# Kernel tuning notes

Hardware: AMD Instinct MI355X
Metric: run time of the kernel (lower is better)

Reference implementation:

```python
import jax, jax.numpy as jnp
import numpy as np

N = 50000
NEG_SLOPE = 0.2


def leaky_relu(x, slope=NEG_SLOPE):
    return jnp.where(x >= 0, x, slope * x)


def gat_conv(x, edge_index, W, a_src, a_dst, bias):
    """PyG GATConv, heads=1, add_self_loops=True.
    x: [N, Fin], edge_index: [2, E] (row 0 = source j, row 1 = target i),
    W: [Fin, Fout], a_src/a_dst: [Fout], bias: [Fout].
    """
    n = x.shape[0]
    # add self loops
    loops = jnp.arange(n, dtype=edge_index.dtype)
    src = jnp.concatenate([edge_index[0], loops])
    dst = jnp.concatenate([edge_index[1], loops])

    xw = x @ W                       # [N, Fout]
    alpha_src = xw @ a_src           # [N]
    alpha_dst = xw @ a_dst           # [N]

    e = leaky_relu(alpha_src[src] + alpha_dst[dst])   # [E+N]
    # segment softmax over edges sharing the same target node
    m = jax.ops.segment_max(e, dst, num_segments=n)   # [N]
    ex = jnp.exp(e - m[dst])
    denom = jax.ops.segment_sum(ex, dst, num_segments=n)  # [N] (>0 via self loops)
    att = ex / denom[dst]                              # [E+N]

    msgs = att[:, None] * xw[src]                      # [E+N, Fout]
    out = jax.ops.segment_sum(msgs, dst, num_segments=n)
    return out + bias


def setup_inputs() -> dict:
    key = jax.random.key(0)
    ks = jax.random.split(key, 12)
    E = 800000
    Fin, H, Fout = 128, 256, 128
    x = jax.random.normal(ks[0], (N, Fin), dtype=jnp.float32)
    edge_index = jax.random.randint(ks[1], (2, E), 0, N, dtype=jnp.int64)
    s = 0.1
    W1 = jax.random.normal(ks[2], (Fin, H), dtype=jnp.float32) * s
    a1_src = jax.random.normal(ks[3], (H,), dtype=jnp.float32) * s
    a1_dst = jax.random.normal(ks[4], (H,), dtype=jnp.float32) * s
    b1 = jax.random.normal(ks[5], (H,), dtype=jnp.float32) * s
    W2 = jax.random.normal(ks[6], (H, Fout), dtype=jnp.float32) * s
    a2_src = jax.random.normal(ks[7], (Fout,), dtype=jnp.float32) * s
    a2_dst = jax.random.normal(ks[8], (Fout,), dtype=jnp.float32) * s
    b2 = jax.random.normal(ks[9], (Fout,), dtype=jnp.float32) * s
    return {"x": x, "edge_index": edge_index, "W1": W1, "a1_src": a1_src,
            "a1_dst": a1_dst, "b1": b1, "W2": W2, "a2_src": a2_src,
            "a2_dst": a2_dst, "b2": b2}


def reference(x, edge_index, W1, a1_src, a1_dst, b1, W2, a2_src, a2_dst, b2):
    h = jax.nn.relu(gat_conv(x, edge_index, W1, a1_src, a1_dst, b1))
    return gat_conv(h, edge_index, W2, a2_src, a2_dst, b2)
```

## Files before the change

### kernel.cpp

```cpp
#include <hip/hip_runtime.h>
#include <hip/hip_bf16.h>

typedef __attribute__((ext_vector_type(8))) short short8;
typedef __attribute__((ext_vector_type(4))) float floatx4;

#define CAP 8192
#define BIN_CH 2048
#define NPB 16

__device__ __forceinline__ float read_f(const void* p, long long i, int fp32m) {
  return fp32m ? ((const float*)p)[i] : (float)((const __hip_bfloat16*)p)[i];
}
__device__ __forceinline__ float bf2f(unsigned short u) {
  return __uint_as_float((unsigned)u << 16);
}
__device__ __forceinline__ unsigned short f2bf(float f) {
  const unsigned u = __float_as_uint(f);
  return (unsigned short)((u + 0x7fffu + ((u >> 16) & 1u)) >> 16);
}

__device__ __forceinline__ void pack_one(const void* W, unsigned short* Wp, int i,
                                         int K, int NOUT, int m) {
  const int k = i / NOUT, n = i - k * NOUT;
  const int ct = n >> 4, c = n & 15, ks = k >> 5, quad = (k >> 3) & 3, j = k & 7;
  Wp[(((ct * (K / 32) + ks) * 4 + quad) * 16 + c) * 8 + j] = f2bf(read_f(W, i, m));
}

__global__ __launch_bounds__(256) void prep_k(const void* __restrict__ x,
                                              const void* __restrict__ ei,
                                              const void* __restrict__ W1,
                                              const void* __restrict__ a1s,
                                              const void* __restrict__ a1d,
                                              const void* __restrict__ b1,
                                              const void* __restrict__ W2,
                                              const void* __restrict__ a2s,
                                              const void* __restrict__ a2d,
                                              const void* __restrict__ b2,
                                              unsigned short* __restrict__ Wp1,
                                              unsigned short* __restrict__ Wp2,
                                              float* __restrict__ w_as1, float* __restrict__ w_ad1,
                                              float* __restrict__ v_a2s, float* __restrict__ v_a2d,
                                              float* __restrict__ v_b1,  float* __restrict__ v_b2,
                                              int* __restrict__ bkcnt,
                                              int* __restrict__ flags) {
  __shared__ int fl_s[2];
  const int t = threadIdx.x, b = blockIdx.x;
  if (t < 64) {
    const unsigned short w = ((const unsigned short*)x)[t * 2];
    const int ef = (w >> 7) & 0xff;
    const bool bf_ok = (ef >= 90 && ef <= 140);
    const unsigned hi = ((const unsigned*)ei)[t * 2 + 1];
    const unsigned long long bm = __ballot(bf_ok);
    const unsigned long long zm = __ballot(hi == 0u);
    if (t == 0) {
      fl_s[0] = (bm == ~0ull) ? 0 : 1;
      fl_s[1] = (zm == ~0ull) ? 1 : 0;
      if (b == 0) { flags[0] = fl_s[0]; flags[1] = fl_s[1]; }
    }
  }
  __syncthreads();
  const int m = fl_s[0];

  if (b < 128) {
    pack_one(W1, Wp1, b * 256 + t, 128, 256, m);
  } else if (b < 256) {
    pack_one(W2, Wp2, (b - 128) * 256 + t, 256, 128, m);
  } else if (b == 256) {
    if (t < 128) {
      float sa = 0.f, sb = 0.f;
      for (int j = 0; j < 256; ++j) {
        const float w = read_f(W1, (long long)t * 256 + j, m);
        sa = fmaf(w, read_f(a1s, j, m), sa);
        sb = fmaf(w, read_f(a1d, j, m), sb);
      }
      w_as1[t] = sa;
      w_ad1[t] = sb;
    }
  } else if (b == 257) {
    if (t < 128) v_a2s[t] = read_f(a2s, t, m);
    else         v_a2d[t - 128] = read_f(a2d, t - 128, m);
  } else if (b == 258) {
    v_b1[t] = read_f(b1, t, m);
  } else {
    if (t < 128) v_b2[t] = read_f(b2, t, m);
    bkcnt[t] = 0;
  }
}

__device__ __forceinline__ void edge_sd(const void* ei, int e, int E, int i64m, int n,
                                        int& s, int& d) {
  if (e < E) {
    if (i64m) { s = (int)((const long long*)ei)[e]; d = (int)((const long long*)ei)[E + e]; }
    else      { s = ((const int*)ei)[e];            d = ((const int*)ei)[E + e]; }
  } else { s = d = e - E; }
  s = min(max(s, 0), n - 1);
  d = min(max(d, 0), n - 1);
}

__global__ __launch_bounds__(256) void front2_k(const void* __restrict__ x,
                                                const void* __restrict__ ei,
                                                const float* __restrict__ w_as1,
                                                const float* __restrict__ w_ad1,
                                                unsigned short* __restrict__ xb,
                                                float* __restrict__ as_, float* __restrict__ ad_,
                                                unsigned* __restrict__ bpool,
                                                int* __restrict__ bkcnt,
                                                int n, int E, int EN, int nbc) {
  __shared__ int fl_s[2];
  __shared__ unsigned stage[BIN_CH];
  __shared__ unsigned daddr[BIN_CH];
  __shared__ int shA[256], shB[256], shC[256], shD[256];
  __shared__ int vtot_s;
  const int t = threadIdx.x, b = blockIdx.x;

  if (t < 64) {
    const unsigned short w = ((const unsigned short*)x)[t * 2];
    const int ef = (w >> 7) & 0xff;
    const bool bf_ok = (ef >= 90 && ef <= 140);
    const unsigned hi = ((const unsigned*)ei)[t * 2 + 1];
    const unsigned long long bm = __ballot(bf_ok);
    const unsigned long long zm = __ballot(hi == 0u);
    if (t == 0) {
      fl_s[0] = (bm == ~0ull) ? 0 : 1;
      fl_s[1] = (zm == ~0ull) ? 1 : 0;
    }
  }
  __syncthreads();
  const int m = fl_s[0], i64m = fl_s[1];

  if (b < nbc) {
    const int gid = b * 256 + t;
    const int node = gid >> 6, lane = gid & 63;
    if (node >= n) return;
    const long long base = (long long)node * 128 + lane * 2;
    const float v0 = read_f(x, base, m), v1 = read_f(x, base + 1, m);
    ushort2 q;
    q.x = f2bf(v0); q.y = f2bf(v1);
    *(ushort2*)(xb + base) = q;
    float s1 = fmaf(v0, w_as1[lane * 2], v1 * w_as1[lane * 2 + 1]);
    float s2 = fmaf(v0, w_ad1[lane * 2], v1 * w_ad1[lane * 2 + 1]);
    for (int off = 32; off; off >>= 1) {
      s1 += __shfl_down(s1, off);
      s2 += __shfl_down(s2, off);
    }
    if (lane == 0) { as_[node] = s1; ad_[node] = s2; }
  } else {
    const int c0 = (b - nbc) * BIN_CH;
    int* bcnt_s = shA; int* boff_s = shB; int* gbase_s = shC; int* sd = shD;
    bcnt_s[t] = 0;
    __syncthreads();

    unsigned val[BIN_CH / 256];
    int buk[BIN_CH / 256];
#pragma unroll
    for (int i = 0; i < BIN_CH / 256; ++i) {
      const int e = c0 + i * 256 + t;
      if (e < EN) {
        int s, d;
        edge_sd(ei, e, E, i64m, n, s, d);
        buk[i] = d >> 8;
        val[i] = (unsigned)s | ((unsigned)(d & 255) << 16);
        atomicAdd(&bcnt_s[buk[i]], 1);
      } else buk[i] = -1;
    }
    __syncthreads();

    const int c = bcnt_s[t];
    sd[t] = c;
    __syncthreads();
    for (int off = 1; off < 256; off <<= 1) {
      const int v = (t >= off) ? sd[t - off] : 0;
      __syncthreads();
      sd[t] += v;
      __syncthreads();
    }
    boff_s[t] = sd[t] - c;
    if (t == 255) vtot_s = sd[255];
    gbase_s[t] = (c > 0) ? atomicAdd(&bkcnt[t], c) : 0;
    bcnt_s[t] = 0;
    __syncthreads();

#pragma unroll
    for (int i = 0; i < BIN_CH / 256; ++i) {
      if (buk[i] >= 0) {
        const int lp = atomicAdd(&bcnt_s[buk[i]], 1);
        const int si = boff_s[buk[i]] + lp;
        stage[si] = val[i];
        const int gp = gbase_s[buk[i]] + lp;
        daddr[si] = (gp < CAP) ? (unsigned)(buk[i] * CAP + gp) : 0xFFFFFFFFu;
      }
    }
    __syncthreads();

    const int vt = vtot_s;
    for (int idx = t; idx < vt; idx += 256)
      if (daddr[idx] != 0xFFFFFFFFu) bpool[daddr[idx]] = stage[idx];
  }
}

__global__ __launch_bounds__(1024) void bucket_csr_k(const unsigned* __restrict__ bpool,
                                                     const int* __restrict__ bkcnt,
                                                     unsigned short* __restrict__ csrc,
                                                     int* __restrict__ start_g,
                                                     int* __restrict__ deg_g, int n) {
  __shared__ int deg_s[256], cur_s[256], sd[256];
  const int t = threadIdx.x, b = blockIdx.x;
  int cnt = bkcnt[b];
  if (cnt > CAP) cnt = CAP;
  if (t < 256) deg_s[t] = 0;
  __syncthreads();
  for (int idx = t; idx < cnt; idx += 1024) {
    const unsigned v = bpool[b * CAP + idx];
    atomicAdd(&deg_s[(v >> 16) & 255], 1);
  }
  __syncthreads();
  const int dg = (t < 256) ? deg_s[t] : 0;
  if (t < 256) sd[t] = dg;
  __syncthreads();
  for (int off = 1; off < 256; off <<= 1) {
    const int v = (t < 256 && t >= off) ? sd[t - off] : 0;
    __syncthreads();
    if (t < 256) sd[t] += v;
    __syncthreads();
  }
  if (t < 256) {
    const int excl = sd[t] - dg;
    const int node = b * 256 + t;
    if (node < n) { start_g[node] = b * CAP + excl; deg_g[node] = dg; }
    cur_s[t] = excl;
  }
  __syncthreads();
  for (int idx = t; idx < cnt; idx += 1024) {
    const unsigned v = bpool[b * CAP + idx];
    const int p = atomicAdd(&cur_s[(v >> 16) & 255], 1);
    csrc[b * CAP + p] = (unsigned short)(v & 0xFFFFu);
  }
}

__device__ __forceinline__ void agg_node(const int start, const int end,
                                         const unsigned short* __restrict__ csrc,
                                         const float* __restrict__ as_, const float adv,
                                         const unsigned short* __restrict__ xw,
                                         const int lane, float* acc) {
  const int slot = lane >> 4, col = lane & 15;
  float dsum = 0.f;
#pragma unroll
  for (int c = 0; c < 8; ++c) acc[c] = 0.f;

  for (int base = start; base < end; base += 64) {
    const int idx = base + lane;
    int s_pre = 0;
    float w_pre = 0.f;
    if (idx < end) {
      s_pre = (int)csrc[idx];
      float v = as_[s_pre] + adv;
      v = (v >= 0.f) ? v : 0.2f * v;
      w_pre = __expf(fminf(v, 60.f));
    }
    dsum += w_pre;
    const int cnt = min(64, end - base);
    for (int j = 0; j < cnt; j += 8) {
      const int jj0 = j + slot, jj1 = j + 4 + slot;
      int s0 = __shfl(s_pre, jj0);
      float w0 = __shfl(w_pre, jj0);
      int s1 = __shfl(s_pre, jj1);
      float w1 = __shfl(w_pre, jj1);
      const bool ok0 = (jj0 < cnt), ok1 = (jj1 < cnt);
      s0 = ok0 ? s0 : 0; w0 = ok0 ? w0 : 0.f;
      s1 = ok1 ? s1 : 0; w1 = ok1 ? w1 : 0.f;
      const short8 q0 = *(const short8*)(xw + (size_t)s0 * 128 + col * 8);
      const short8 q1 = *(const short8*)(xw + (size_t)s1 * 128 + col * 8);
#pragma unroll
      for (int c = 0; c < 8; ++c) {
        acc[c] = fmaf(w0, bf2f((unsigned short)q0[c]), acc[c]);
        acc[c] = fmaf(w1, bf2f((unsigned short)q1[c]), acc[c]);
      }
    }
  }
  for (int off = 32; off; off >>= 1) dsum += __shfl_down(dsum, off);
  dsum = __shfl(dsum, 0);
  const float r = 1.f / fmaxf(dsum, 1e-30f);
#pragma unroll
  for (int c = 0; c < 8; ++c) {
    acc[c] += __shfl_xor(acc[c], 16);
    acc[c] += __shfl_xor(acc[c], 32);
    acc[c] *= r;
  }
}

#define LSTR 136
#define HSTR 264
__global__ __launch_bounds__(256, 8) void agg_gemm12_k(const int* __restrict__ start_g,
                                                       const int* __restrict__ deg_g,
                                                       const unsigned short* __restrict__ csrc,
                                                       const float* __restrict__ as_,
                                                       const float* __restrict__ ad_,
                                                       const unsigned short* __restrict__ xb,
                                                       const unsigned short* __restrict__ Wp1,
                                                       const unsigned short* __restrict__ Wp2,
                                                       const float* __restrict__ v_b1,
                                                       const float* __restrict__ v_a2s,
                                                       const float* __restrict__ v_a2d,
                                                       unsigned short* __restrict__ xw2,
                                                       float* __restrict__ as2,
                                                       float* __restrict__ ad2, int n) {
  __shared__ unsigned short lds[NPB * LSTR];
  __shared__ unsigned short hs[NPB * HSTR];
  __shared__ float al_s[NPB], al_d[NPB];
  const int wv = threadIdx.x >> 6, lane = threadIdx.x & 63;
  const int slot = lane >> 4, col = lane & 15;
  const int node0 = blockIdx.x * NPB;

  for (int k = 0; k < 4; ++k) {
    const int rv = wv * 4 + k;
    const int node = node0 + rv;
    float acc[8];
    if (node < n) {
      const int start = start_g[node];
      agg_node(start, start + deg_g[node], csrc, as_, ad_[node], xb, lane, acc);
    } else {
#pragma unroll
      for (int c = 0; c < 8; ++c) acc[c] = 0.f;
    }
    if (slot == 0) {
      short8 q;
#pragma unroll
      for (int c = 0; c < 8; ++c) q[c] = (short)f2bf(acc[c]);
      *(short8*)&lds[rv * LSTR + col * 8] = q;
    }
  }
  if (threadIdx.x < NPB) { al_s[threadIdx.x] = 0.f; al_d[threadIdx.x] = 0.f; }
  __syncthreads();

  const int quad = slot, c = col;
  short8 af1[4];
#pragma unroll
  for (int ks = 0; ks < 4; ++ks)
    af1[ks] = *(const short8*)&lds[c * LSTR + ks * 32 + quad * 8];
#pragma unroll
  for (int j = 0; j < 4; ++j) {
    const int ct = wv * 4 + j;
    floatx4 g = {0.f, 0.f, 0.f, 0.f};
#pragma unroll
    for (int ks = 0; ks < 4; ++ks) {
      const short8 bf = *(const short8*)(Wp1 + (size_t)((ct * 4 + ks) * 64 + lane) * 8);
      g = __builtin_amdgcn_mfma_f32_16x16x32_bf16(af1[ks], bf, g, 0, 0, 0);
    }
    const float bv = v_b1[ct * 16 + c];
#pragma unroll
    for (int r = 0; r < 4; ++r) {
      const float v = g[r] + bv;
      hs[(quad * 4 + r) * HSTR + ct * 16 + c] = f2bf(v > 0.f ? v : 0.f);
    }
  }
  __syncthreads();

#pragma unroll
  for (int j2 = 0; j2 < 2; ++j2) {
    const int ct = wv * 2 + j2;
    floatx4 a2 = {0.f, 0.f, 0.f, 0.f};
#pragma unroll
    for (int ks = 0; ks < 8; ++ks) {
      const short8 af = *(const short8*)&hs[c * HSTR + ks * 32 + quad * 8];
      const short8 bf = *(const short8*)(Wp2 + (size_t)((ct * 8 + ks) * 64 + lane) * 8);
      a2 = __builtin_amdgcn_mfma_f32_16x16x32_bf16(af, bf, a2, 0, 0, 0);
    }
    const float asv = v_a2s[ct * 16 + c], adv = v_a2d[ct * 16 + c];
    float pa_s[4], pa_d[4];
#pragma unroll
    for (int r = 0; r < 4; ++r) {
      pa_s[r] = a2[r] * asv;
      pa_d[r] = a2[r] * adv;
      const int rr = node0 + quad * 4 + r;
      if (rr < n) xw2[(size_t)rr * 128 + ct * 16 + c] = f2bf(a2[r]);
    }
    for (int off = 1; off < 16; off <<= 1) {
#pragma unroll
      for (int r = 0; r < 4; ++r) {
        pa_s[r] += __shfl_xor(pa_s[r], off);
        pa_d[r] += __shfl_xor(pa_d[r], off);
      }
    }
    if (c == 0) {
#pragma unroll
      for (int r = 0; r < 4; ++r) {
        atomicAdd(&al_s[quad * 4 + r], pa_s[r]);
        atomicAdd(&al_d[quad * 4 + r], pa_d[r]);
      }
    }
  }
  __syncthreads();
  if (threadIdx.x < NPB) {
    const int rr = node0 + threadIdx.x;
    if (rr < n) { as2[rr] = al_s[threadIdx.x]; ad2[rr] = al_d[threadIdx.x]; }
  }
}

__global__ __launch_bounds__(256, 8) void agg_out_k(const int* __restrict__ start_g,
                                                    const int* __restrict__ deg_g,
                                                    const unsigned short* __restrict__ csrc,
                                                    const float* __restrict__ as_,
                                                    const float* __restrict__ ad_,
                                                    const unsigned short* __restrict__ xw,
                                                    const float* __restrict__ bias,
                                                    void* __restrict__ outp, int n,
                                                    const int* __restrict__ flags) {
  const int wv = threadIdx.x >> 6, lane = threadIdx.x & 63;
  const int slot = lane >> 4, col = lane & 15;
  const int node0 = blockIdx.x * 16;
  const int fm = flags[0];
  for (int k = 0; k < 4; ++k) {
    const int node = node0 + wv * 4 + k;
    if (node >= n) continue;
    const int start = start_g[node];
    float acc[8];
    agg_node(start, start + deg_g[node], csrc, as_, ad_[node], xw, lane, acc);
    if (slot == 0) {
      const int c0 = col * 8;
      if (fm) {
        float* o = (float*)outp + (size_t)node * 128 + c0;
        floatx4 q0, q1;
#pragma unroll
        for (int c = 0; c < 4; ++c) {
          q0[c] = acc[c] + bias[c0 + c];
          q1[c] = acc[c + 4] + bias[c0 + 4 + c];
        }
        *(floatx4*)o = q0;
        *(floatx4*)(o + 4) = q1;
      } else {
        short8 q;
#pragma unroll
        for (int c = 0; c < 8; ++c) q[c] = (short)f2bf(acc[c] + bias[c0 + c]);
        *(short8*)((unsigned short*)outp + (size_t)node * 128 + c0) = q;
      }
    }
  }
}

extern "C" void kernel_launch(void* const* d_in, const int* in_sizes, int n_in,
                              void* d_out, int out_size, void* d_ws, size_t ws_size,
                              hipStream_t stream) {
  const void* x   = d_in[0];
  const void* ei  = d_in[1];
  const void* W1  = d_in[2];
  const void* a1s = d_in[3];
  const void* a1d = d_in[4];
  const void* b1  = d_in[5];
  const void* W2  = d_in[6];
  const void* a2s = d_in[7];
  const void* a2d = d_in[8];
  const void* b2  = d_in[9];

  const int N  = in_sizes[0] / 128;
  const int E  = in_sizes[1] / 2;
  const int EN = E + N;
  const int NBUK = (N + 255) / 256;

  unsigned short* B1 = (unsigned short*)d_ws;
  unsigned short* H  = B1 + (size_t)N * 128;
  unsigned short* xw2 = H;
  float* as2 = (float*)(H + (size_t)N * 128);
  float* ad2 = as2 + N;
  float* as_   = (float*)(H + (size_t)N * 256);
  float* ad_   = as_ + N;
  int*   start_g = (int*)(ad_ + N);
  int*   deg_g   = start_g + N;
  int*   bkcnt   = deg_g + N;
  unsigned* bpool = (unsigned*)(bkcnt + 256);
  unsigned short* csrc = (unsigned short*)(bpool + (size_t)NBUK * CAP);
  unsigned short* Wp1 = csrc + (size_t)NBUK * CAP;
  unsigned short* Wp2 = Wp1 + 128 * 256;
  float* vecs  = (float*)(Wp2 + 256 * 128);
  int*   flags = (int*)(vecs + 1152);
  float* w_as1 = vecs,        *w_ad1 = vecs + 128;
  float* v_a2s = vecs + 256,  *v_a2d = vecs + 384;
  float* v_b1  = vecs + 512,  *v_b2  = vecs + 768;

  const int NB = (N * 64 + 255) / 256;
  const int BB = (EN + BIN_CH - 1) / BIN_CH;
  const int AG = (N + NPB - 1) / NPB;

  prep_k<<<260, 256, 0, stream>>>(x, ei, W1, a1s, a1d, b1, W2, a2s, a2d, b2,
                                  Wp1, Wp2, w_as1, w_ad1, v_a2s, v_a2d, v_b1, v_b2,
                                  bkcnt, flags);

  front2_k<<<NB + BB, 256, 0, stream>>>(x, ei, w_as1, w_ad1, B1, as_, ad_,
                                        bpool, bkcnt, N, E, EN, NB);

  bucket_csr_k<<<NBUK, 1024, 0, stream>>>(bpool, bkcnt, csrc, start_g, deg_g, N);

  agg_gemm12_k<<<AG, 256, 0, stream>>>(start_g, deg_g, csrc, as_, ad_, B1, Wp1, Wp2,
                                       v_b1, v_a2s, v_a2d, xw2, as2, ad2, N);

  agg_out_k<<<AG, 256, 0, stream>>>(start_g, deg_g, csrc, as2, ad2, xw2, v_b2, d_out, N, flags);
}
```

Baseline: 247.5 us.

## Precompute layer-1 attention weights in CSR build and pack into 32-bit entries

The CSR build kernel now computes each edge's layer-1 leaky-ReLU/exp attention weight and packs it as bf16 next to the 16-bit local source index in one 32-bit CSR entry. It also accumulates the per-node softmax denominator and stores its reciprocal. This removes the per-edge alpha gather, exp and cross-lane denominator reduction from the layer-1 aggregation loop. Layer-2 aggregation reads the same packed array, ignores the stored weight, and repacks its own weights for the shuffle. The cost is twice the CSR index bandwidth, extra work in the bucket kernel, and attention weights rounded to bf16.

```diff
diff --git a/kernel.cpp b/kernel.cpp
--- a/kernel.cpp
+++ b/kernel.cpp
@@ -200,14 +200,18 @@
 
 __global__ __launch_bounds__(1024) void bucket_csr_k(const unsigned* __restrict__ bpool,
                                                      const int* __restrict__ bkcnt,
-                                                     unsigned short* __restrict__ csrc,
+                                                     const float* __restrict__ as_,
+                                                     const float* __restrict__ ad_,
+                                                     unsigned* __restrict__ csr32,
                                                      int* __restrict__ start_g,
-                                                     int* __restrict__ deg_g, int n) {
+                                                     int* __restrict__ deg_g,
+                                                     float* __restrict__ r1_g, int n) {
   __shared__ int deg_s[256], cur_s[256], sd[256];
+  __shared__ float dsum_s[256];
   const int t = threadIdx.x, b = blockIdx.x;
   int cnt = bkcnt[b];
   if (cnt > CAP) cnt = CAP;
-  if (t < 256) deg_s[t] = 0;
+  if (t < 256) { deg_s[t] = 0; dsum_s[t] = 0.f; }
   __syncthreads();
   for (int idx = t; idx < cnt; idx += 1024) {
     const unsigned v = bpool[b * CAP + idx];
@@ -232,42 +236,92 @@
   __syncthreads();
   for (int idx = t; idx < cnt; idx += 1024) {
     const unsigned v = bpool[b * CAP + idx];
-    const int p = atomicAdd(&cur_s[(v >> 16) & 255], 1);
-    csrc[b * CAP + p] = (unsigned short)(v & 0xFFFFu);
-  }
-}
-
-__device__ __forceinline__ void agg_node(const int start, const int end,
-                                         const unsigned short* __restrict__ csrc,
-                                         const float* __restrict__ as_, const float adv,
-                                         const unsigned short* __restrict__ xw,
-                                         const int lane, float* acc) {
+    const int dl = (v >> 16) & 255;
+    const int s = (int)(v & 0xFFFFu);
+    float val = as_[s] + ad_[b * 256 + dl];
+    val = (val >= 0.f) ? val : 0.2f * val;
+    const float w = __expf(fminf(val, 60.f));
+    const unsigned short wb = f2bf(w);
+    atomicAdd(&dsum_s[dl], bf2f(wb));
+    const int p = atomicAdd(&cur_s[dl], 1);
+    csr32[b * CAP + p] = (unsigned)s | ((unsigned)wb << 16);
+  }
+  __syncthreads();
+  if (t < 256) {
+    const int node = b * 256 + t;
+    if (node < n) r1_g[node] = 1.f / fmaxf(dsum_s[t], 1e-30f);
+  }
+}
+
+__device__ __forceinline__ void agg_node_w(const int start, const int end,
+                                           const unsigned* __restrict__ csr32,
+                                           const unsigned short* __restrict__ xw,
+                                           const int lane, const float rnorm, float* acc) {
   const int slot = lane >> 4, col = lane & 15;
-  float dsum = 0.f;
 #pragma unroll
   for (int c = 0; c < 8; ++c) acc[c] = 0.f;
 
   for (int base = start; base < end; base += 64) {
     const int idx = base + lane;
-    int s_pre = 0;
-    float w_pre = 0.f;
-    if (idx < end) {
-      s_pre = (int)csrc[idx];
-      float v = as_[s_pre] + adv;
-      v = (v >= 0.f) ? v : 0.2f * v;
-      w_pre = __expf(fminf(v, 60.f));
-    }
-    dsum += w_pre;
+    const unsigned e_pre = (idx < end) ? csr32[idx] : 0u;
     const int cnt = min(64, end - base);
     for (int j = 0; j < cnt; j += 8) {
       const int jj0 = j + slot, jj1 = j + 4 + slot;
-      int s0 = __shfl(s_pre, jj0);
-      float w0 = __shfl(w_pre, jj0);
-      int s1 = __shfl(s_pre, jj1);
-      float w1 = __shfl(w_pre, jj1);
-      const bool ok0 = (jj0 < cnt), ok1 = (jj1 < cnt);
-      s0 = ok0 ? s0 : 0; w0 = ok0 ? w0 : 0.f;
-      s1 = ok1 ? s1 : 0; w1 = ok1 ? w1 : 0.f;
+      unsigned e0 = (unsigned)__shfl((int)e_pre, jj0);
+      unsigned e1 = (unsigned)__shfl((int)e_pre, jj1);
+      e0 = (jj0 < cnt) ? e0 : 0u;
+      e1 = (jj1 < cnt) ? e1 : 0u;
+      const int s0 = (int)(e0 & 0xFFFFu), s1 = (int)(e1 & 0xFFFFu);
+      const float w0 = bf2f((unsigned short)(e0 >> 16));
+      const float w1 = bf2f((unsigned short)(e1 >> 16));
+      const short8 q0 = *(const short8*)(xw + (size_t)s0 * 128 + col * 8);
+      const short8 q1 = *(const short8*)(xw + (size_t)s1 * 128 + col * 8);
+#pragma unroll
+      for (int c = 0; c < 8; ++c) {
+        acc[c] = fmaf(w0, bf2f((unsigned short)q0[c]), acc[c]);
+        acc[c] = fmaf(w1, bf2f((unsigned short)q1[c]), acc[c]);
+      }
+    }
+  }
+#pragma unroll
+  for (int c = 0; c < 8; ++c) {
+    acc[c] += __shfl_xor(acc[c], 16);
+    acc[c] += __shfl_xor(acc[c], 32);
+    acc[c] *= rnorm;
+  }
+}
+
+__device__ __forceinline__ void agg_node2(const int start, const int end,
+                                          const unsigned* __restrict__ csr32,
+                                          const float* __restrict__ as2, const float adv,
+                                          const unsigned short* __restrict__ xw,
+                                          const int lane, float* acc) {
+  const int slot = lane >> 4, col = lane & 15;
+  float dsum = 0.f;
+#pragma unroll
+  for (int c = 0; c < 8; ++c) acc[c] = 0.f;
+
+  for (int base = start; base < end; base += 64) {
+    const int idx = base + lane;
+    unsigned p_pre = 0u;
+    if (idx < end) {
+      const int s = (int)(csr32[idx] & 0xFFFFu);
+      float v = as2[s] + adv;
+      v = (v >= 0.f) ? v : 0.2f * v;
+      const unsigned short wb = f2bf(__expf(fminf(v, 60.f)));
+      dsum += bf2f(wb);
+      p_pre = (unsigned)s | ((unsigned)wb << 16);
+    }
+    const int cnt = min(64, end - base);
+    for (int j = 0; j < cnt; j += 8) {
+      const int jj0 = j + slot, jj1 = j + 4 + slot;
+      unsigned e0 = (unsigned)__shfl((int)p_pre, jj0);
+      unsigned e1 = (unsigned)__shfl((int)p_pre, jj1);
+      e0 = (jj0 < cnt) ? e0 : 0u;
+      e1 = (jj1 < cnt) ? e1 : 0u;
+      const int s0 = (int)(e0 & 0xFFFFu), s1 = (int)(e1 & 0xFFFFu);
+      const float w0 = bf2f((unsigned short)(e0 >> 16));
+      const float w1 = bf2f((unsigned short)(e1 >> 16));
       const short8 q0 = *(const short8*)(xw + (size_t)s0 * 128 + col * 8);
       const short8 q1 = *(const short8*)(xw + (size_t)s1 * 128 + col * 8);
 #pragma unroll
@@ -292,9 +346,8 @@
 #define HSTR 264
 __global__ __launch_bounds__(256, 8) void agg_gemm12_k(const int* __restrict__ start_g,
                                                        const int* __restrict__ deg_g,
-                                                       const unsigned short* __restrict__ csrc,
-                                                       const float* __restrict__ as_,
-                                                       const float* __restrict__ ad_,
+                                                       const unsigned* __restrict__ csr32,
+                                                       const float* __restrict__ r1_g,
                                                        const unsigned short* __restrict__ xb,
                                                        const unsigned short* __restrict__ Wp1,
                                                        const unsigned short* __restrict__ Wp2,
@@ -317,7 +370,7 @@
     float acc[8];
     if (node < n) {
       const int start = start_g[node];
-      agg_node(start, start + deg_g[node], csrc, as_, ad_[node], xb, lane, acc);
+      agg_node_w(start, start + deg_g[node], csr32, xb, lane, r1_g[node], acc);
     } else {
 #pragma unroll
       for (int c = 0; c < 8; ++c) acc[c] = 0.f;
@@ -398,9 +451,9 @@
 
 __global__ __launch_bounds__(256, 8) void agg_out_k(const int* __restrict__ start_g,
                                                     const int* __restrict__ deg_g,
-                                                    const unsigned short* __restrict__ csrc,
-                                                    const float* __restrict__ as_,
-                                                    const float* __restrict__ ad_,
+                                                    const unsigned* __restrict__ csr32,
+                                                    const float* __restrict__ as2,
+                                                    const float* __restrict__ ad2,
                                                     const unsigned short* __restrict__ xw,
                                                     const float* __restrict__ bias,
                                                     void* __restrict__ outp, int n,
@@ -414,7 +467,7 @@
     if (node >= n) continue;
     const int start = start_g[node];
     float acc[8];
-    agg_node(start, start + deg_g[node], csrc, as_, ad_[node], xw, lane, acc);
+    agg_node2(start, start + deg_g[node], csr32, as2, ad2[node], xw, lane, acc);
     if (slot == 0) {
       const int c0 = col * 8;
       if (fm) {
@@ -461,14 +514,15 @@
   unsigned short* xw2 = H;
   float* as2 = (float*)(H + (size_t)N * 128);
   float* ad2 = as2 + N;
+  unsigned* csr32 = (unsigned*)(ad2 + N);
   float* as_   = (float*)(H + (size_t)N * 256);
   float* ad_   = as_ + N;
   int*   start_g = (int*)(ad_ + N);
   int*   deg_g   = start_g + N;
-  int*   bkcnt   = deg_g + N;
+  float* r1_g    = (float*)(deg_g + N);
+  int*   bkcnt   = (int*)(r1_g + N);
   unsigned* bpool = (unsigned*)(bkcnt + 256);
-  unsigned short* csrc = (unsigned short*)(bpool + (size_t)NBUK * CAP);
-  unsigned short* Wp1 = csrc + (size_t)NBUK * CAP;
+  unsigned short* Wp1 = (unsigned short*)(bpool + (size_t)NBUK * CAP);
   unsigned short* Wp2 = Wp1 + 128 * 256;
   float* vecs  = (float*)(Wp2 + 256 * 128);
   int*   flags = (int*)(vecs + 1152);
@@ -487,10 +541,12 @@
   front2_k<<<NB + BB, 256, 0, stream>>>(x, ei, w_as1, w_ad1, B1, as_, ad_,
                                         bpool, bkcnt, N, E, EN, NB);
 
-  bucket_csr_k<<<NBUK, 1024, 0, stream>>>(bpool, bkcnt, csrc, start_g, deg_g, N);
-
-  agg_gemm12_k<<<AG, 256, 0, stream>>>(start_g, deg_g, csrc, as_, ad_, B1, Wp1, Wp2,
+  bucket_csr_k<<<NBUK, 1024, 0, stream>>>(bpool, bkcnt, as_, ad_, csr32,
+                                          start_g, deg_g, r1_g, N);
+
+  agg_gemm12_k<<<AG, 256, 0, stream>>>(start_g, deg_g, csr32, r1_g, B1, Wp1, Wp2,
                                        v_b1, v_a2s, v_a2d, xw2, as2, ad2, N);
 
-  agg_out_k<<<AG, 256, 0, stream>>>(start_g, deg_g, csrc, as2, ad2, xw2, v_b2, d_out, N, flags);
-}
+  agg_out_k<<<AG, 256, 0, stream>>>(start_g, deg_g, csr32, as2, ad2, xw2, v_b2,
+                                    d_out, N, flags);
+}
```

Result: faster. 241.9 us (-2.2%).
